# Kernel optimization log

Hardware: AMD Instinct MI355X
Metric: run time of the kernel (lower is better)

The kernel has to match this reference:

```python
import jax, jax.numpy as jnp
import numpy as np

D_MODEL = 1024
NUM_HEADS = 16
D_K = D_MODEL // NUM_HEADS  # 64
THETA = 10000.0


def setup_inputs() -> dict:
    key = jax.random.key(0)
    ks = jax.random.split(key, 5)
    B, S = 4, 2048
    scale = D_MODEL ** -0.5  # keep logits in a sane range (params are uninit in source)
    x = jax.random.normal(ks[0], (B, S, D_MODEL), jnp.float32)
    W_q = jax.random.normal(ks[1], (D_MODEL, D_MODEL), jnp.float32) * scale
    W_k = jax.random.normal(ks[2], (D_MODEL, D_MODEL), jnp.float32) * scale
    W_v = jax.random.normal(ks[3], (D_MODEL, D_MODEL), jnp.float32) * scale
    W_o = jax.random.normal(ks[4], (D_MODEL, D_MODEL), jnp.float32) * scale
    token_positions = jnp.arange(S, dtype=jnp.int64) if jax.config.jax_enable_x64 else jnp.arange(S, dtype=jnp.int32)
    return {"x": x, "W_q": W_q, "W_k": W_k, "W_v": W_v, "W_o": W_o,
            "token_positions": token_positions}


def _rope(x, positions):
    # x: [..., S, D_K]; interleaved-pair rotation, matching the torch RoPE:
    # pairs (x[2i], x[2i+1]) rotated by angle pos * inv_freq[i].
    inv_freq = 1.0 / (THETA ** (jnp.arange(0, D_K, 2, dtype=jnp.float32) / D_K))  # [D_K//2]
    ang = positions.astype(jnp.float32)[:, None] * inv_freq[None, :]  # [S, D_K//2]
    cos, sin = jnp.cos(ang), jnp.sin(ang)
    x0, x1 = x[..., 0::2], x[..., 1::2]
    r0 = cos * x0 - sin * x1
    r1 = sin * x0 + cos * x1
    return jnp.stack([r0, r1], axis=-1).reshape(x.shape)


def reference(x, W_q, W_k, W_v, W_o, token_positions):
    B, S, _ = x.shape
    def proj(W):  # einsum '... s d, D d -> ... s D' == x @ W.T
        return (x @ W.T).reshape(B, S, NUM_HEADS, D_K).transpose(0, 2, 1, 3)  # [B,H,S,D_K]
    Q = _rope(proj(W_q), token_positions)
    K = _rope(proj(W_k), token_positions)
    V = proj(W_v)
    scores = jnp.einsum('bhqd,bhkd->bhqk', Q, K) / jnp.sqrt(jnp.float32(D_K))
    causal = jnp.tril(jnp.ones((S, S), dtype=bool))
    scores = jnp.where(causal, scores, -jnp.inf)
    A = jax.nn.softmax(scores, axis=-1)
    out = jnp.einsum('bhqk,bhkd->bhqd', A, V)            # [B,H,S,D_K]
    out = out.transpose(0, 2, 1, 3).reshape(B, S, D_MODEL)
    return out @ W_o.T
```

## Files before the change

### kernel.cpp

```cpp
#include <hip/hip_runtime.h>
#include <hip/hip_bf16.h>


typedef _Float16 half4_t __attribute__((ext_vector_type(4)));
typedef _Float16 half8_t __attribute__((ext_vector_type(8)));
typedef float    floatx4 __attribute__((ext_vector_type(4)));

constexpr int Bn = 4, Sn = 2048, Dm = 1024, Hn = 16, Dk = 64;
constexpr int Mtot = Bn * Sn;

__global__ __launch_bounds__(256)
void cvt_f16(const float* __restrict__ in, _Float16* __restrict__ out, int n)
{
    int i = (blockIdx.x * 256 + threadIdx.x) * 8;
    if (i >= n) return;
    float4 a = *(const float4*)(in + i);
    float4 b = *(const float4*)(in + i + 4);
    half8_t h;
    h[0] = (_Float16)a.x; h[1] = (_Float16)a.y;
    h[2] = (_Float16)a.z; h[3] = (_Float16)a.w;
    h[4] = (_Float16)b.x; h[5] = (_Float16)b.y;
    h[6] = (_Float16)b.z; h[7] = (_Float16)b.w;
    *(half8_t*)(out + i) = h;
}

__global__ __launch_bounds__(256)
void proj_qkv(const _Float16* __restrict__ xh,
              const _Float16* __restrict__ Wqh,
              const _Float16* __restrict__ Wkh,
              const _Float16* __restrict__ Wvh,
              _Float16* __restrict__ outb,
              const int* __restrict__ pos)
{
    __shared__ _Float16 As[128][72];
    __shared__ _Float16 Bs[128][72];

    const int z = blockIdx.z;
    const _Float16* W = (z == 0) ? Wqh : (z == 1) ? Wkh : Wvh;
    _Float16* out = outb + (size_t)z * (size_t)Bn * Hn * Sn * Dk;

    const int tid = threadIdx.x, lane = tid & 63, w = tid >> 6;
    const int h = lane >> 4, lid = lane & 15;
    const int wm = (w >> 1) * 64, wn = (w & 1) * 64;
    const int m0 = blockIdx.y * 128, n0 = blockIdx.x * 128;
    const int sr = tid >> 1, sc = (tid & 1) * 32;

    const _Float16* Ap = xh + (size_t)(m0 + sr) * Dm + sc;
    const _Float16* Wp = W + (size_t)(n0 + sr) * Dm + sc;

    half8_t pa[4], pb[4];
    #pragma unroll
    for (int u = 0; u < 4; ++u) {
        pa[u] = *(const half8_t*)(Ap + 8 * u);
        pb[u] = *(const half8_t*)(Wp + 8 * u);
    }
    floatx4 acc[4][4] = {};

    for (int k0 = 0; k0 < Dm; k0 += 64) {
        __syncthreads();
        #pragma unroll
        for (int u = 0; u < 4; ++u) {
            *(half8_t*)&As[sr][sc + 8 * u] = pa[u];
            *(half8_t*)&Bs[sr][sc + 8 * u] = pb[u];
        }
        __syncthreads();
        if (k0 + 64 < Dm) {
            #pragma unroll
            for (int u = 0; u < 4; ++u) {
                pa[u] = *(const half8_t*)(Ap + k0 + 64 + 8 * u);
                pb[u] = *(const half8_t*)(Wp + k0 + 64 + 8 * u);
            }
        }
        #pragma unroll
        for (int kk = 0; kk < 2; ++kk) {
            half8_t af[4], bf[4];
            #pragma unroll
            for (int i = 0; i < 4; ++i) {
                af[i] = *(const half8_t*)&As[wm + 16 * i + lid][kk * 32 + 8 * h];
                bf[i] = *(const half8_t*)&Bs[wn + 16 * i + lid][kk * 32 + 8 * h];
            }
            #pragma unroll
            for (int i = 0; i < 4; ++i)
                #pragma unroll
                for (int j = 0; j < 4; ++j)
                    acc[i][j] = __builtin_amdgcn_mfma_f32_16x16x32_f16(
                        af[i], bf[j], acc[i][j], 0, 0, 0);
        }
    }

    const bool rope = (z < 2);
    #pragma unroll
    for (int j = 0; j < 4; ++j) {
        const int n = n0 + wn + 16 * j + lid;
        const int hd = n >> 6, d = n & 63;
        float invf = 0.f;
        if (rope)
            invf = __powf(10000.0f, -(float)(d & ~1) * (1.0f / 64.0f));
        #pragma unroll
        for (int i = 0; i < 4; ++i)
            #pragma unroll
            for (int r = 0; r < 4; ++r) {
                const int m = m0 + wm + 16 * i + 4 * h + r;
                const int bb = m >> 11, s = m & (Sn - 1);
                float val = acc[i][j][r];
                float o = val;
                if (rope) {
                    float part = __shfl_xor(val, 1);
                    float ang = (float)pos[s] * invf;
                    float sv, cv;
                    __sincosf(ang, &sv, &cv);
                    o = (d & 1) ? (sv * part + cv * val)
                                : (cv * val - sv * part);
                }
                out[((size_t)(bb * Hn + hd) * Sn + s) * Dk + d] = (_Float16)o;
            }
    }
}

__global__ __launch_bounds__(256)
void gemm_out(const _Float16* __restrict__ Ah, const _Float16* __restrict__ Wh,
              float* __restrict__ out)
{
    __shared__ _Float16 As[128][72];
    __shared__ _Float16 Bs[128][72];

    const int tid = threadIdx.x, lane = tid & 63, w = tid >> 6;
    const int h = lane >> 4, lid = lane & 15;
    const int wm = (w >> 1) * 64, wn = (w & 1) * 64;
    const int m0 = blockIdx.y * 128, n0 = blockIdx.x * 128;
    const int sr = tid >> 1, sc = (tid & 1) * 32;

    const _Float16* Ap = Ah + (size_t)(m0 + sr) * Dm + sc;
    const _Float16* Wp = Wh + (size_t)(n0 + sr) * Dm + sc;

    half8_t pa[4], pb[4];
    #pragma unroll
    for (int u = 0; u < 4; ++u) {
        pa[u] = *(const half8_t*)(Ap + 8 * u);
        pb[u] = *(const half8_t*)(Wp + 8 * u);
    }
    floatx4 acc[4][4] = {};

    for (int k0 = 0; k0 < Dm; k0 += 64) {
        __syncthreads();
        #pragma unroll
        for (int u = 0; u < 4; ++u) {
            *(half8_t*)&As[sr][sc + 8 * u] = pa[u];
            *(half8_t*)&Bs[sr][sc + 8 * u] = pb[u];
        }
        __syncthreads();
        if (k0 + 64 < Dm) {
            #pragma unroll
            for (int u = 0; u < 4; ++u) {
                pa[u] = *(const half8_t*)(Ap + k0 + 64 + 8 * u);
                pb[u] = *(const half8_t*)(Wp + k0 + 64 + 8 * u);
            }
        }
        #pragma unroll
        for (int kk = 0; kk < 2; ++kk) {
            half8_t af[4], bf[4];
            #pragma unroll
            for (int i = 0; i < 4; ++i) {
                af[i] = *(const half8_t*)&As[wm + 16 * i + lid][kk * 32 + 8 * h];
                bf[i] = *(const half8_t*)&Bs[wn + 16 * i + lid][kk * 32 + 8 * h];
            }
            #pragma unroll
            for (int i = 0; i < 4; ++i)
                #pragma unroll
                for (int j = 0; j < 4; ++j)
                    acc[i][j] = __builtin_amdgcn_mfma_f32_16x16x32_f16(
                        af[i], bf[j], acc[i][j], 0, 0, 0);
        }
    }

    #pragma unroll
    for (int i = 0; i < 4; ++i)
        #pragma unroll
        for (int j = 0; j < 4; ++j) {
            const int n = n0 + wn + 16 * j + lid;
            #pragma unroll
            for (int r = 0; r < 4; ++r) {
                const int m = m0 + wm + 16 * i + 4 * h + r;
                out[(size_t)m * Dm + n] = acc[i][j][r];
            }
        }
}

__global__ __launch_bounds__(512)
void flash_f16(const _Float16* __restrict__ Qg, const _Float16* __restrict__ Kg,
               const _Float16* __restrict__ Vg, _Float16* __restrict__ AO)
{
    __shared__ _Float16 Ks[2][64][72];
    __shared__ _Float16 VT[2][64][72];

    const int tid = threadIdx.x, lane = tid & 63, w = tid >> 6;
    const int h = lane >> 4, lid = lane & 15;
    const int qt = (int)gridDim.x - 1 - (int)blockIdx.x;
    const int head = blockIdx.y, b = blockIdx.z;
    const int q0 = qt * 128;
    const size_t base = (size_t)(b * Hn + head) * Sn * Dk;

    const int wq = q0 + 16 * w + lid;
    const half8_t qf0 = *(const half8_t*)(Qg + base + (size_t)wq * Dk + 8 * h);
    const half8_t qf1 = *(const half8_t*)(Qg + base + (size_t)wq * Dk + 32 + 8 * h);

    const int nt = 2 * qt + 2;
    const int sr = tid >> 3, sj = tid & 7;
    const _Float16* Kp = Kg + base + (size_t)sr * Dk + 8 * sj;
    const _Float16* Vp = Vg + base + (size_t)sr * Dk + 8 * sj;

    {
        half8_t k0v = *(const half8_t*)(Kp);
        half8_t v0v = *(const half8_t*)(Vp);
        *(half8_t*)&Ks[0][sr][8 * sj] = k0v;
        #pragma unroll
        for (int e = 0; e < 8; ++e) {
            int ee = (e + sj) & 7;
            VT[0][8 * sj + ee][sr] = v0v[ee];
        }
    }
    __syncthreads();

    float m_r = -1e30f, l_r = 0.f;
    floatx4 accO[4] = {};

    for (int t = 0; t < nt; ++t) {
        const int cur = t & 1;
        half8_t kn, vn;
        const bool more = (t + 1 < nt);
        if (more) {
            kn = *(const half8_t*)(Kp + (size_t)(t + 1) * 64 * Dk);
            vn = *(const half8_t*)(Vp + (size_t)(t + 1) * 64 * Dk);
        }

        const int k0 = t * 64;
        const bool active = (k0 <= q0 + 16 * w + 15);
        if (active) {
            floatx4 sac[4] = {};
            #pragma unroll
            for (int tt = 0; tt < 4; ++tt) {
                half8_t kf0 = *(const half8_t*)&Ks[cur][16 * tt + lid][8 * h];
                half8_t kf1 = *(const half8_t*)&Ks[cur][16 * tt + lid][32 + 8 * h];
                sac[tt] = __builtin_amdgcn_mfma_f32_16x16x32_f16(kf0, qf0, sac[tt], 0, 0, 0);
                sac[tt] = __builtin_amdgcn_mfma_f32_16x16x32_f16(kf1, qf1, sac[tt], 0, 0, 0);
            }
            const bool needmask = (k0 + 63 > q0 + 16 * w);
            #pragma unroll
            for (int tt = 0; tt < 4; ++tt)
                #pragma unroll
                for (int r = 0; r < 4; ++r) {
                    float x = sac[tt][r] * 0.125f;
                    if (needmask && (k0 + 16 * tt + 4 * h + r > wq)) x = -1e30f;
                    sac[tt][r] = x;
                }
            float pm = -1e30f;
            #pragma unroll
            for (int tt = 0; tt < 4; ++tt)
                #pragma unroll
                for (int r = 0; r < 4; ++r) pm = fmaxf(pm, sac[tt][r]);
            pm = fmaxf(pm, __shfl_xor(pm, 16));
            pm = fmaxf(pm, __shfl_xor(pm, 32));
            const float nm = fmaxf(m_r, pm);
            const float sc = __expf(m_r - nm);
            float rs = 0.f;
            half8_t pf0, pf1;
            #pragma unroll
            for (int tt = 0; tt < 4; ++tt)
                #pragma unroll
                for (int r = 0; r < 4; ++r) {
                    float p = __expf(sac[tt][r] - nm);
                    rs += p;
                    if (tt < 2) pf0[(tt & 1) * 4 + r] = (_Float16)p;
                    else        pf1[(tt & 1) * 4 + r] = (_Float16)p;
                }
            rs += __shfl_xor(rs, 16);
            rs += __shfl_xor(rs, 32);
            l_r = l_r * sc + rs;
            m_r = nm;
            #pragma unroll
            for (int dt = 0; dt < 4; ++dt) accO[dt] *= sc;
            #pragma unroll
            for (int dt = 0; dt < 4; ++dt) {
                half4_t a0 = *(const half4_t*)&VT[cur][16 * dt + lid][4 * h];
                half4_t a1 = *(const half4_t*)&VT[cur][16 * dt + lid][16 + 4 * h];
                half8_t vf0 = __builtin_shufflevector(a0, a1, 0, 1, 2, 3, 4, 5, 6, 7);
                accO[dt] = __builtin_amdgcn_mfma_f32_16x16x32_f16(vf0, pf0, accO[dt], 0, 0, 0);
                half4_t b0 = *(const half4_t*)&VT[cur][16 * dt + lid][32 + 4 * h];
                half4_t b1 = *(const half4_t*)&VT[cur][16 * dt + lid][48 + 4 * h];
                half8_t vf1 = __builtin_shufflevector(b0, b1, 0, 1, 2, 3, 4, 5, 6, 7);
                accO[dt] = __builtin_amdgcn_mfma_f32_16x16x32_f16(vf1, pf1, accO[dt], 0, 0, 0);
            }
        }

        if (more) {
            *(half8_t*)&Ks[cur ^ 1][sr][8 * sj] = kn;
            #pragma unroll
            for (int e = 0; e < 8; ++e) {
                int ee = (e + sj) & 7;
                VT[cur ^ 1][8 * sj + ee][sr] = vn[ee];
            }
        }
        __syncthreads();
    }

    const float inv = 1.0f / l_r;
    #pragma unroll
    for (int dt = 0; dt < 4; ++dt)
        #pragma unroll
        for (int r = 0; r < 4; ++r) {
            const int d = 16 * dt + 4 * h + r;
            AO[((size_t)(b * Sn + wq)) * Dm + head * Dk + d] =
                (_Float16)(accO[dt][r] * inv);
        }
}

extern "C" void kernel_launch(void* const* d_in, const int* in_sizes, int n_in,
                              void* d_out, int out_size, void* d_ws, size_t ws_size,
                              hipStream_t stream)
{
    (void)in_sizes; (void)n_in; (void)out_size; (void)ws_size;
    const float* x  = (const float*)d_in[0];
    const float* Wq = (const float*)d_in[1];
    const float* Wk = (const float*)d_in[2];
    const float* Wv = (const float*)d_in[3];
    const float* Wo = (const float*)d_in[4];
    const int*  pos = (const int*)d_in[5];
    float* out = (float*)d_out;

    const size_t nX = (size_t)Mtot * Dm;
    const size_t nW = (size_t)Dm * Dm;
    const size_t perBuf = (size_t)Bn * Hn * Sn * Dk;

    _Float16* xh  = (_Float16*)d_ws;
    _Float16* Wqh = xh + nX;
    _Float16* Wkh = Wqh + nW;
    _Float16* Wvh = Wkh + nW;
    _Float16* Woh = Wvh + nW;
    _Float16* Qh  = Woh + nW;
    _Float16* AOh = Qh + 3 * perBuf;

    dim3 blk(256);
    hipLaunchKernelGGL(cvt_f16, dim3((int)(nX / 2048)), blk, 0, stream, x, xh, (int)nX);
    hipLaunchKernelGGL(cvt_f16, dim3((int)(nW / 2048)), blk, 0, stream, Wq, Wqh, (int)nW);
    hipLaunchKernelGGL(cvt_f16, dim3((int)(nW / 2048)), blk, 0, stream, Wk, Wkh, (int)nW);
    hipLaunchKernelGGL(cvt_f16, dim3((int)(nW / 2048)), blk, 0, stream, Wv, Wvh, (int)nW);
    hipLaunchKernelGGL(cvt_f16, dim3((int)(nW / 2048)), blk, 0, stream, Wo, Woh, (int)nW);

    dim3 gp(Dm / 128, Mtot / 128, 3);
    hipLaunchKernelGGL(proj_qkv, gp, blk, 0, stream, xh, Wqh, Wkh, Wvh, Qh, pos);

    dim3 fg(Sn / 128, Hn, Bn);
    hipLaunchKernelGGL(flash_f16, fg, dim3(512), 0, stream,
                       Qh, Qh + perBuf, Qh + 2 * perBuf, AOh);

    dim3 gg(Dm / 128, Mtot / 128);
    hipLaunchKernelGGL(gemm_out, gg, blk, 0, stream, AOh, Woh, out);
}
```

Baseline: 399.6 us.

## Pair causal query tiles per block and streamline softmax with exp2 and lazy rescale

Each flash block now handles two query tiles, pr and 15-pr, so every block does the same causal work and the grid is halved. The softmax folds the 1/sqrt(d)·log2(e) scale into Q in fp16 and uses exp2f. It skips rescaling the accumulator unless the running max grows by more than 8, and packs probabilities with cvt_pkrtz. The costs are fewer blocks (512) on the GPU, a small precision loss from pre-scaling Q in fp16, and p values that can grow up to 2^8 before conversion.

```diff
diff --git a/kernel.cpp b/kernel.cpp
--- a/kernel.cpp
+++ b/kernel.cpp
@@ -2,9 +2,14 @@
 #include <hip/hip_bf16.h>
 
 
+typedef _Float16 half2_t __attribute__((ext_vector_type(2)));
 typedef _Float16 half4_t __attribute__((ext_vector_type(4)));
 typedef _Float16 half8_t __attribute__((ext_vector_type(8)));
 typedef float    floatx4 __attribute__((ext_vector_type(4)));
+
+__device__ __forceinline__ half2_t cvtpk(float a, float b) {
+    return __builtin_bit_cast(half2_t, __builtin_amdgcn_cvt_pkrtz(a, b));
+}
 
 constexpr int Bn = 4, Sn = 2048, Dm = 1024, Hn = 16, Dk = 64;
 constexpr int Mtot = Bn * Sn;
@@ -195,123 +200,146 @@
 
     const int tid = threadIdx.x, lane = tid & 63, w = tid >> 6;
     const int h = lane >> 4, lid = lane & 15;
-    const int qt = (int)gridDim.x - 1 - (int)blockIdx.x;
+    const int pr = blockIdx.x;
     const int head = blockIdx.y, b = blockIdx.z;
-    const int q0 = qt * 128;
     const size_t base = (size_t)(b * Hn + head) * Sn * Dk;
 
-    const int wq = q0 + 16 * w + lid;
-    const half8_t qf0 = *(const half8_t*)(Qg + base + (size_t)wq * Dk + 8 * h);
-    const half8_t qf1 = *(const half8_t*)(Qg + base + (size_t)wq * Dk + 32 + 8 * h);
-
-    const int nt = 2 * qt + 2;
     const int sr = tid >> 3, sj = tid & 7;
     const _Float16* Kp = Kg + base + (size_t)sr * Dk + 8 * sj;
     const _Float16* Vp = Vg + base + (size_t)sr * Dk + 8 * sj;
 
-    {
-        half8_t k0v = *(const half8_t*)(Kp);
-        half8_t v0v = *(const half8_t*)(Vp);
-        *(half8_t*)&Ks[0][sr][8 * sj] = k0v;
-        #pragma unroll
-        for (int e = 0; e < 8; ++e) {
-            int ee = (e + sj) & 7;
-            VT[0][8 * sj + ee][sr] = v0v[ee];
-        }
-    }
-    __syncthreads();
-
-    float m_r = -1e30f, l_r = 0.f;
-    floatx4 accO[4] = {};
-
-    for (int t = 0; t < nt; ++t) {
-        const int cur = t & 1;
-        half8_t kn, vn;
-        const bool more = (t + 1 < nt);
-        if (more) {
-            kn = *(const half8_t*)(Kp + (size_t)(t + 1) * 64 * Dk);
-            vn = *(const half8_t*)(Vp + (size_t)(t + 1) * 64 * Dk);
-        }
-
-        const int k0 = t * 64;
-        const bool active = (k0 <= q0 + 16 * w + 15);
-        if (active) {
-            floatx4 sac[4] = {};
-            #pragma unroll
-            for (int tt = 0; tt < 4; ++tt) {
-                half8_t kf0 = *(const half8_t*)&Ks[cur][16 * tt + lid][8 * h];
-                half8_t kf1 = *(const half8_t*)&Ks[cur][16 * tt + lid][32 + 8 * h];
-                sac[tt] = __builtin_amdgcn_mfma_f32_16x16x32_f16(kf0, qf0, sac[tt], 0, 0, 0);
-                sac[tt] = __builtin_amdgcn_mfma_f32_16x16x32_f16(kf1, qf1, sac[tt], 0, 0, 0);
-            }
-            const bool needmask = (k0 + 63 > q0 + 16 * w);
-            #pragma unroll
-            for (int tt = 0; tt < 4; ++tt)
-                #pragma unroll
-                for (int r = 0; r < 4; ++r) {
-                    float x = sac[tt][r] * 0.125f;
-                    if (needmask && (k0 + 16 * tt + 4 * h + r > wq)) x = -1e30f;
-                    sac[tt][r] = x;
-                }
-            float pm = -1e30f;
-            #pragma unroll
-            for (int tt = 0; tt < 4; ++tt)
-                #pragma unroll
-                for (int r = 0; r < 4; ++r) pm = fmaxf(pm, sac[tt][r]);
-            pm = fmaxf(pm, __shfl_xor(pm, 16));
-            pm = fmaxf(pm, __shfl_xor(pm, 32));
-            const float nm = fmaxf(m_r, pm);
-            const float sc = __expf(m_r - nm);
-            float rs = 0.f;
-            half8_t pf0, pf1;
-            #pragma unroll
-            for (int tt = 0; tt < 4; ++tt)
-                #pragma unroll
-                for (int r = 0; r < 4; ++r) {
-                    float p = __expf(sac[tt][r] - nm);
-                    rs += p;
-                    if (tt < 2) pf0[(tt & 1) * 4 + r] = (_Float16)p;
-                    else        pf1[(tt & 1) * 4 + r] = (_Float16)p;
-                }
-            rs += __shfl_xor(rs, 16);
-            rs += __shfl_xor(rs, 32);
-            l_r = l_r * sc + rs;
-            m_r = nm;
-            #pragma unroll
-            for (int dt = 0; dt < 4; ++dt) accO[dt] *= sc;
-            #pragma unroll
-            for (int dt = 0; dt < 4; ++dt) {
-                half4_t a0 = *(const half4_t*)&VT[cur][16 * dt + lid][4 * h];
-                half4_t a1 = *(const half4_t*)&VT[cur][16 * dt + lid][16 + 4 * h];
-                half8_t vf0 = __builtin_shufflevector(a0, a1, 0, 1, 2, 3, 4, 5, 6, 7);
-                accO[dt] = __builtin_amdgcn_mfma_f32_16x16x32_f16(vf0, pf0, accO[dt], 0, 0, 0);
-                half4_t b0 = *(const half4_t*)&VT[cur][16 * dt + lid][32 + 4 * h];
-                half4_t b1 = *(const half4_t*)&VT[cur][16 * dt + lid][48 + 4 * h];
-                half8_t vf1 = __builtin_shufflevector(b0, b1, 0, 1, 2, 3, 4, 5, 6, 7);
-                accO[dt] = __builtin_amdgcn_mfma_f32_16x16x32_f16(vf1, pf1, accO[dt], 0, 0, 0);
-            }
-        }
-
-        if (more) {
-            *(half8_t*)&Ks[cur ^ 1][sr][8 * sj] = kn;
+    const _Float16 qsc = (_Float16)0.18033688f;
+
+    #pragma unroll 1
+    for (int seg = 0; seg < 2; ++seg) {
+        const int qt = (seg == 0) ? pr : (15 - pr);
+        const int q0 = qt * 128;
+        const int wq = q0 + 16 * w + lid;
+
+        half8_t qf0 = *(const half8_t*)(Qg + base + (size_t)wq * Dk + 8 * h);
+        half8_t qf1 = *(const half8_t*)(Qg + base + (size_t)wq * Dk + 32 + 8 * h);
+        qf0 *= qsc;
+        qf1 *= qsc;
+
+        const int nt = 2 * qt + 2;
+
+        {
+            half8_t k0v = *(const half8_t*)(Kp);
+            half8_t v0v = *(const half8_t*)(Vp);
+            *(half8_t*)&Ks[0][sr][8 * sj] = k0v;
             #pragma unroll
             for (int e = 0; e < 8; ++e) {
                 int ee = (e + sj) & 7;
-                VT[cur ^ 1][8 * sj + ee][sr] = vn[ee];
-            }
-        }
-        __syncthreads();
-    }
-
-    const float inv = 1.0f / l_r;
-    #pragma unroll
-    for (int dt = 0; dt < 4; ++dt)
-        #pragma unroll
-        for (int r = 0; r < 4; ++r) {
-            const int d = 16 * dt + 4 * h + r;
-            AO[((size_t)(b * Sn + wq)) * Dm + head * Dk + d] =
-                (_Float16)(accO[dt][r] * inv);
-        }
+                VT[0][8 * sj + ee][sr] = v0v[ee];
+            }
+        }
+        __syncthreads();
+
+        float m_r = -1e30f, l_r = 0.f;
+        floatx4 accO[4] = {};
+
+        for (int t = 0; t < nt; ++t) {
+            const int cur = t & 1;
+            half8_t kn, vn;
+            const bool more = (t + 1 < nt);
+            if (more) {
+                kn = *(const half8_t*)(Kp + (size_t)(t + 1) * 64 * Dk);
+                vn = *(const half8_t*)(Vp + (size_t)(t + 1) * 64 * Dk);
+            }
+
+            const int k0 = t * 64;
+            const bool active = (k0 <= q0 + 16 * w + 15);
+            if (active) {
+                floatx4 sac[4] = {};
+                #pragma unroll
+                for (int tt = 0; tt < 4; ++tt) {
+                    half8_t kf0 = *(const half8_t*)&Ks[cur][16 * tt + lid][8 * h];
+                    half8_t kf1 = *(const half8_t*)&Ks[cur][16 * tt + lid][32 + 8 * h];
+                    sac[tt] = __builtin_amdgcn_mfma_f32_16x16x32_f16(kf0, qf0, sac[tt], 0, 0, 0);
+                    sac[tt] = __builtin_amdgcn_mfma_f32_16x16x32_f16(kf1, qf1, sac[tt], 0, 0, 0);
+                }
+                if (k0 + 63 > q0 + 16 * w) {
+                    #pragma unroll
+                    for (int tt = 0; tt < 4; ++tt)
+                        #pragma unroll
+                        for (int r = 0; r < 4; ++r)
+                            if (k0 + 16 * tt + 4 * h + r > wq) sac[tt][r] = -1e30f;
+                }
+                float pm = -1e30f;
+                #pragma unroll
+                for (int tt = 0; tt < 4; ++tt)
+                    #pragma unroll
+                    for (int r = 0; r < 4; ++r) pm = fmaxf(pm, sac[tt][r]);
+                pm = fmaxf(pm, __shfl_xor(pm, 16));
+                pm = fmaxf(pm, __shfl_xor(pm, 32));
+                if (!__all(pm - m_r <= 8.0f)) {
+                    const float nm = fmaxf(m_r, pm);
+                    const float sc = exp2f(m_r - nm);
+                    l_r *= sc;
+                    #pragma unroll
+                    for (int dt = 0; dt < 4; ++dt) accO[dt] *= sc;
+                    m_r = nm;
+                }
+                float pv[16], rs = 0.f;
+                #pragma unroll
+                for (int tt = 0; tt < 4; ++tt)
+                    #pragma unroll
+                    for (int r = 0; r < 4; ++r) {
+                        float p = exp2f(sac[tt][r] - m_r);
+                        rs += p;
+                        pv[4 * tt + r] = p;
+                    }
+                rs += __shfl_xor(rs, 16);
+                rs += __shfl_xor(rs, 32);
+                l_r += rs;
+                half2_t c0 = cvtpk(pv[0], pv[1]);
+                half2_t c1 = cvtpk(pv[2], pv[3]);
+                half2_t c2 = cvtpk(pv[4], pv[5]);
+                half2_t c3 = cvtpk(pv[6], pv[7]);
+                half2_t c4 = cvtpk(pv[8], pv[9]);
+                half2_t c5 = cvtpk(pv[10], pv[11]);
+                half2_t c6 = cvtpk(pv[12], pv[13]);
+                half2_t c7 = cvtpk(pv[14], pv[15]);
+                half4_t l0 = __builtin_shufflevector(c0, c1, 0, 1, 2, 3);
+                half4_t l1 = __builtin_shufflevector(c2, c3, 0, 1, 2, 3);
+                half4_t l2 = __builtin_shufflevector(c4, c5, 0, 1, 2, 3);
+                half4_t l3 = __builtin_shufflevector(c6, c7, 0, 1, 2, 3);
+                half8_t pf0 = __builtin_shufflevector(l0, l1, 0, 1, 2, 3, 4, 5, 6, 7);
+                half8_t pf1 = __builtin_shufflevector(l2, l3, 0, 1, 2, 3, 4, 5, 6, 7);
+                #pragma unroll
+                for (int dt = 0; dt < 4; ++dt) {
+                    half4_t a0 = *(const half4_t*)&VT[cur][16 * dt + lid][4 * h];
+                    half4_t a1 = *(const half4_t*)&VT[cur][16 * dt + lid][16 + 4 * h];
+                    half8_t vf0 = __builtin_shufflevector(a0, a1, 0, 1, 2, 3, 4, 5, 6, 7);
+                    accO[dt] = __builtin_amdgcn_mfma_f32_16x16x32_f16(vf0, pf0, accO[dt], 0, 0, 0);
+                    half4_t b0 = *(const half4_t*)&VT[cur][16 * dt + lid][32 + 4 * h];
+                    half4_t b1 = *(const half4_t*)&VT[cur][16 * dt + lid][48 + 4 * h];
+                    half8_t vf1 = __builtin_shufflevector(b0, b1, 0, 1, 2, 3, 4, 5, 6, 7);
+                    accO[dt] = __builtin_amdgcn_mfma_f32_16x16x32_f16(vf1, pf1, accO[dt], 0, 0, 0);
+                }
+            }
+
+            if (more) {
+                *(half8_t*)&Ks[cur ^ 1][sr][8 * sj] = kn;
+                #pragma unroll
+                for (int e = 0; e < 8; ++e) {
+                    int ee = (e + sj) & 7;
+                    VT[cur ^ 1][8 * sj + ee][sr] = vn[ee];
+                }
+            }
+            __syncthreads();
+        }
+
+        const float inv = 1.0f / l_r;
+        #pragma unroll
+        for (int dt = 0; dt < 4; ++dt)
+            #pragma unroll
+            for (int r = 0; r < 4; ++r) {
+                const int d = 16 * dt + 4 * h + r;
+                AO[((size_t)(b * Sn + wq)) * Dm + head * Dk + d] =
+                    (_Float16)(accO[dt][r] * inv);
+            }
+    }
 }
 
 extern "C" void kernel_launch(void* const* d_in, const int* in_sizes, int n_in,
@@ -349,7 +377,7 @@
     dim3 gp(Dm / 128, Mtot / 128, 3);
     hipLaunchKernelGGL(proj_qkv, gp, blk, 0, stream, xh, Wqh, Wkh, Wvh, Qh, pos);
 
-    dim3 fg(Sn / 128, Hn, Bn);
+    dim3 fg(Sn / 256, Hn, Bn);
     hipLaunchKernelGGL(flash_f16, fg, dim3(512), 0, stream,
                        Qh, Qh + perBuf, Qh + 2 * perBuf, AOh);
 
```

After: 325.2 us. 1.23x faster.
